# Kernel tuning notes

Hardware: AMD Instinct MI355X
Metric: run time of the kernel (lower is better)

Reference implementation:

```python
import jax, jax.numpy as jnp
import numpy as np


def _conv1x1(x, W, b):
    # 1x1 conv == per-pixel channel matmul: x [B,C,H,W], W [O,C], b [O]
    return jnp.einsum('bchw,oc->bohw', x, W) + b[None, :, None, None]


def setup_inputs() -> dict:
    key = jax.random.key(0)
    ks = jax.random.split(key, 9)
    B, C, H, W = 16, 512, 32, 32
    s = 1.0 / np.sqrt(C)
    inp = {
        'x': jax.random.normal(ks[0], (B, C, H, W), dtype=jnp.float32),
        'Wq': jax.random.normal(ks[1], (C, C), dtype=jnp.float32) * s,
        'bq': jax.random.normal(ks[2], (C,), dtype=jnp.float32) * 0.01,
        'Wk': jax.random.normal(ks[3], (C, C), dtype=jnp.float32) * s,
        'bk': jax.random.normal(ks[4], (C,), dtype=jnp.float32) * 0.01,
        'Wv': jax.random.normal(ks[5], (C, C), dtype=jnp.float32) * s,
        'bv': jax.random.normal(ks[6], (C,), dtype=jnp.float32) * 0.01,
        'Wo': jax.random.normal(ks[7], (C, C), dtype=jnp.float32) * s,
        'bo': jax.random.normal(ks[8], (C,), dtype=jnp.float32) * 0.01,
    }
    return inp


def reference(x, Wq, bq, Wk, bk, Wv, bv, Wo, bo):
    B, C, H, W = x.shape
    q = _conv1x1(x, Wq, bq)
    k = _conv1x1(x, Wk, bk)
    v = _conv1x1(x, Wv, bv)
    hw = H * W
    qf = q.reshape(B, C, hw)  # [B,C,HW]
    kf = k.reshape(B, C, hw)
    vf = v.reshape(B, C, hw)
    # scores[b,i,j] = sum_c q[b,c,i] * k[b,c,j], scaled by c^-0.5
    scores = jnp.einsum('bci,bcj->bij', qf, kf) * (C ** -0.5)
    attn = jax.nn.softmax(scores, axis=2)  # softmax over keys j
    # out[b,c,i] = sum_j v[b,c,j] * attn[b,i,j]
    out = jnp.einsum('bcj,bij->bci', vf, attn).reshape(B, C, H, W)
    out = _conv1x1(out, Wo, bo)
    return x + out
```

## Files before the change

### kernel.cpp

```cpp
#include <hip/hip_runtime.h>
#include <hip/hip_bf16.h>
#include <math.h>


typedef __bf16 bf16x8 __attribute__((ext_vector_type(8)));
typedef float  f32x16 __attribute__((ext_vector_type(16)));

__device__ __forceinline__ unsigned short f2bf(float f) {
    unsigned u = __float_as_uint(f);
    u += 0x7fff + ((u >> 16) & 1);
    return (unsigned short)(u >> 16);
}

__device__ __forceinline__ void gload_lds16(const void* g, void* l) {
    __builtin_amdgcn_global_load_lds(
        (const __attribute__((address_space(1))) void*)g,
        (__attribute__((address_space(3))) void*)l, 16, 0, 0);
}

struct GemmP {
    const unsigned short* A;
    const unsigned short* B;
    void* C;
    const float* bias;
    const float* resid;
    float* lsum;
    int M, N, K, ldA, ldB;
    long sA, sB, sC, sR;
    int ln_nn, ln_pb;
    float scale;
};

template<bool OUT_F32, int BIAS_MODE, bool RESID, int EXPM>
__device__ __forceinline__ void gemm_body(const GemmP p, int L,
                                          unsigned short* Als,
                                          unsigned short* Bls)
{
    const int xcd = L & 7;
    const int idx = L >> 3;
    const int bz  = xcd * 2 + (idx >> p.ln_pb);
    const int w   = idx & ((1 << p.ln_pb) - 1);
    const int m0  = (w >> p.ln_nn) << 7;
    const int n0  = (w & ((1 << p.ln_nn) - 1)) << 7;

    const unsigned short* A = p.A + bz * p.sA;
    const unsigned short* B = p.B + bz * p.sB;

    const int tid  = threadIdx.x;
    const int lane = tid & 63;
    const int wave = tid >> 6;
    const int wm   = wave >> 1;
    const int wn   = wave & 1;

    const int ar = lane >> 2;
    const int ak = (((lane & 3) ^ ((ar >> 1) & 3))) * 8;

    const unsigned short* agp = A + (long)(m0 + wave * 16 + ar) * p.ldA + ak;
    const unsigned short* bgp = B + (long)(n0 + wave * 16 + ar) * p.ldB + ak;
    const long aj = 64L * p.ldA;
    const long bj = 64L * p.ldB;

    unsigned short* al0  = Als + wave * 512;
    unsigned short* al0h = Als + (wave + 4) * 512;
    unsigned short* al1  = Als + 4096 + wave * 512;
    unsigned short* al1h = Als + 4096 + (wave + 4) * 512;
    unsigned short* bl0  = Bls + wave * 512;
    unsigned short* bl0h = Bls + (wave + 4) * 512;
    unsigned short* bl1  = Bls + 4096 + wave * 512;
    unsigned short* bl1h = Bls + 4096 + (wave + 4) * 512;

    const int ln31 = lane & 31;
    const int hi   = lane >> 5;
    const int swz  = ((ln31 >> 1) & 3) << 3;

    f32x16 acc[2][2] = {};

    for (int k0 = 0; k0 < p.K; k0 += 64) {
        gload_lds16(agp,           al0);
        gload_lds16(agp + aj,      al0h);
        gload_lds16(agp + 32,      al1);
        gload_lds16(agp + 32 + aj, al1h);
        gload_lds16(bgp,           bl0);
        gload_lds16(bgp + bj,      bl0h);
        gload_lds16(bgp + 32,      bl1);
        gload_lds16(bgp + 32 + bj, bl1h);
        agp += 64; bgp += 64;
        __syncthreads();

        #pragma unroll
        for (int pp = 0; pp < 2; ++pp) {
            const unsigned short* Ap = Als + pp * 4096;
            const unsigned short* Bp = Bls + pp * 4096;
            bf16x8 af[2][2], bfr[2][2];
            #pragma unroll
            for (int mt = 0; mt < 2; ++mt)
                #pragma unroll
                for (int ks = 0; ks < 2; ++ks)
                    af[mt][ks] = *(const bf16x8*)
                        &Ap[(wm * 64 + mt * 32 + ln31) * 32 +
                            ((ks * 16 + hi * 8) ^ swz)];
            #pragma unroll
            for (int nt = 0; nt < 2; ++nt)
                #pragma unroll
                for (int ks = 0; ks < 2; ++ks)
                    bfr[nt][ks] = *(const bf16x8*)
                        &Bp[(wn * 64 + nt * 32 + ln31) * 32 +
                            ((ks * 16 + hi * 8) ^ swz)];

            #pragma unroll
            for (int ks = 0; ks < 2; ++ks)
                #pragma unroll
                for (int mt = 0; mt < 2; ++mt)
                    #pragma unroll
                    for (int nt = 0; nt < 2; ++nt)
                        acc[mt][nt] = __builtin_amdgcn_mfma_f32_32x32x16_bf16(
                            af[mt][ks], bfr[nt][ks], acc[mt][nt], 0, 0, 0);
        }
        __syncthreads();
    }

    float* Cf = (float*)p.C + bz * p.sC;
    unsigned short* Ch = (unsigned short*)p.C + bz * p.sC;
    const float* resid = RESID ? (p.resid + bz * p.sR) : nullptr;
    const int N = p.N;

    if (EXPM == 1) {
        float* lrow = p.lsum + bz * (long)p.M;
        #pragma unroll
        for (int mt = 0; mt < 2; ++mt) {
            #pragma unroll
            for (int r = 0; r < 16; ++r) {
                const int row = m0 + wm * 64 + mt * 32 +
                                (r & 3) + 8 * (r >> 2) + 4 * hi;
                float rs = 0.0f;
                #pragma unroll
                for (int nt = 0; nt < 2; ++nt) {
                    const int col = n0 + wn * 64 + nt * 32 + ln31;
                    const float e = __expf(acc[mt][nt][r] * p.scale);
                    rs += e;
                    Ch[(long)row * N + col] = f2bf(e);
                }
                rs += __shfl_xor(rs, 1);
                rs += __shfl_xor(rs, 2);
                rs += __shfl_xor(rs, 4);
                rs += __shfl_xor(rs, 8);
                rs += __shfl_xor(rs, 16);
                if (ln31 == 0) atomicAdd(&lrow[row], rs);
            }
        }
    } else {
        #pragma unroll
        for (int mt = 0; mt < 2; ++mt) {
            float linv[16];
            if (EXPM == 2) {
                const float* lrow = p.lsum + bz * (long)p.M;
                #pragma unroll
                for (int r = 0; r < 16; ++r)
                    linv[r] = 1.0f / lrow[m0 + wm * 64 + mt * 32 +
                                          (r & 3) + 8 * (r >> 2) + 4 * hi];
            }
            #pragma unroll
            for (int nt = 0; nt < 2; ++nt) {
                const int col = n0 + wn * 64 + nt * 32 + ln31;
                const float bn = (BIAS_MODE == 2) ? p.bias[col] : 0.0f;
                #pragma unroll
                for (int r = 0; r < 16; ++r) {
                    const int row = m0 + wm * 64 + mt * 32 +
                                    (r & 3) + 8 * (r >> 2) + 4 * hi;
                    float val = acc[mt][nt][r] + bn;
                    if (BIAS_MODE == 1) val += p.bias[row];
                    if (EXPM == 2) val *= linv[r];
                    const long o = (long)row * N + col;
                    if (RESID) val += resid[o];
                    if (OUT_F32) Cf[o] = val;
                    else         Ch[o] = f2bf(val);
                }
            }
        }
    }
}

template<bool OUT_F32, int BIAS_MODE, bool RESID, int EXPM>
__global__ __launch_bounds__(256) void gemm_bt_mfma(GemmP p)
{
    __shared__ unsigned short Als[2 * 4096];
    __shared__ unsigned short Bls[2 * 4096];
    gemm_body<OUT_F32, BIAS_MODE, RESID, EXPM>(p, blockIdx.x, Als, Bls);
}

__global__ __launch_bounds__(256) void gemm_qkv_fused(GemmP pqk, GemmP pv, int split)
{
    __shared__ unsigned short Als[2 * 4096];
    __shared__ unsigned short Bls[2 * 4096];
    if ((int)blockIdx.x < split)
        gemm_body<false, 2, false, 0>(pqk, blockIdx.x, Als, Bls);
    else
        gemm_body<false, 1, false, 0>(pv, blockIdx.x - split, Als, Bls);
}

__global__ __launch_bounds__(256) void prep_all(
    const float* __restrict__ x, unsigned short* __restrict__ xT,
    const float* __restrict__ Wq, const float* __restrict__ Wk,
    const float* __restrict__ Wv, const float* __restrict__ Wo,
    const float* __restrict__ bq, const float* __restrict__ bk,
    unsigned short* __restrict__ Wb, float* __restrict__ biasqk,
    float* __restrict__ lsum)
{
    const int b = blockIdx.x;
    const int t = threadIdx.x;
    if (b < 8192) {
        __shared__ float tl[32][33];
        const int batch = b >> 9;
        const int rem = b & 511;
        const int p0 = (rem & 31) * 32;
        const int c0 = (rem >> 5) * 32;
        const float* xb = x + (long)batch * 524288;
        unsigned short* xTb = xT + (long)batch * 524288;
        const int tx = t & 31;
        const int ty = t >> 5;
        #pragma unroll
        for (int i = 0; i < 4; ++i)
            tl[ty + 8 * i][tx] = xb[(long)(c0 + ty + 8 * i) * 1024 + p0 + tx];
        __syncthreads();
        #pragma unroll
        for (int i = 0; i < 4; ++i)
            xTb[(long)(p0 + ty + 8 * i) * 512 + c0 + tx] = f2bf(tl[tx][ty + 8 * i]);
    } else if (b < 9216) {
        const int wb = b - 8192;
        const float* srcs[4] = {Wq, Wk, Wv, Wo};
        const float* s = srcs[wb >> 8];
        unsigned short* d = Wb + (long)(wb >> 8) * 262144;
        const int i = ((wb & 255) * 256 + t) * 4;
        const float4 f = *(const float4*)(s + i);
        ushort4 h;
        h.x = f2bf(f.x); h.y = f2bf(f.y); h.z = f2bf(f.z); h.w = f2bf(f.w);
        *(ushort4*)(d + i) = h;
    } else {
        biasqk[t]       = bq[t];
        biasqk[256 + t] = bq[256 + t];
        biasqk[512 + t] = bk[t];
        biasqk[768 + t] = bk[256 + t];
        #pragma unroll
        for (int i = 0; i < 64; ++i) lsum[i * 256 + t] = 0.0f;
    }
}

extern "C" void kernel_launch(void* const* d_in, const int* in_sizes, int n_in,
                              void* d_out, int out_size, void* d_ws, size_t ws_size,
                              hipStream_t stream)
{
    const float* x  = (const float*)d_in[0];
    const float* Wq = (const float*)d_in[1];
    const float* bq = (const float*)d_in[2];
    const float* Wk = (const float*)d_in[3];
    const float* bk = (const float*)d_in[4];
    const float* Wv = (const float*)d_in[5];
    const float* bv = (const float*)d_in[6];
    const float* Wo = (const float*)d_in[7];
    const float* bo = (const float*)d_in[8];
    float* out = (float*)d_out;

    const int Bn = 16, C = 512, HW = 1024;
    const long CHW = (long)C * HW;
    const long SHW = (long)HW * HW;

    unsigned short* xT   = (unsigned short*)d_ws;
    unsigned short* qkT  = xT + Bn * CHW;
    unsigned short* vB   = qkT + Bn * SHW;
    unsigned short* expS = vB + Bn * CHW;
    unsigned short* Wb   = expS + Bn * SHW;
    float* biasqk = (float*)(Wb + 4 * 262144);
    float* lsum   = biasqk + 1024;
    unsigned short* OT = xT;

    unsigned short* Wvb = Wb + 2 * 262144;
    unsigned short* Wob = Wb + 3 * 262144;

    const dim3 blk(256);
    const float scale = 0.044194173824159216f;

    prep_all<<<dim3(9217), blk, 0, stream>>>(x, xT, Wq, Wk, Wv, Wo, bq, bk,
                                             Wb, biasqk, lsum);

    GemmP pqk = { xT, Wb, qkT, biasqk, nullptr, nullptr,
                  HW, 2 * C, C, C, C, CHW, 0, SHW, 0, 3, 6, 0.0f };
    GemmP pv  = { Wvb, xT, vB, bv, nullptr, nullptr,
                  C, HW, C, C, C, 0, CHW, CHW, 0, 3, 5, 0.0f };
    gemm_qkv_fused<<<dim3(1536), blk, 0, stream>>>(pqk, pv, 1024);

    GemmP ps  = { qkT, qkT + C, expS, nullptr, nullptr, lsum,
                  HW, HW, C, 2 * C, 2 * C, SHW, SHW, SHW, 0, 3, 6, scale };
    gemm_bt_mfma<false, 0, false, 1><<<dim3(1024), blk, 0, stream>>>(ps);

    GemmP po  = { expS, vB, OT, nullptr, nullptr, lsum,
                  HW, C, HW, HW, HW, SHW, CHW, CHW, 0, 2, 5, 0.0f };
    gemm_bt_mfma<false, 0, false, 2><<<dim3(512), blk, 0, stream>>>(po);

    GemmP pout = { Wob, OT, out, bo, x, nullptr,
                   C, HW, C, C, C, 0, CHW, CHW, CHW, 3, 5, 0.0f };
    gemm_bt_mfma<true, 1, true, 0><<<dim3(512), blk, 0, stream>>>(pout);
}
```

Baseline: 227.0 us.

## Double-buffer LDS tiles to overlap global loads with MFMA compute

Replaces the load-then-compute loop over 64-wide K chunks with a ping-pong pipeline over 32-wide K chunks using the two LDS halves as buffers. The next chunk's global-to-LDS loads are issued before computing on the current one, so memory latency can hide behind MFMA work. The number of barriers per K element stays the same, but each step does half as much compute per barrier. The loop assumes K is a multiple of 64.

```diff
diff --git a/kernel.cpp b/kernel.cpp
--- a/kernel.cpp
+++ b/kernel.cpp
@@ -60,62 +60,64 @@
     const long aj = 64L * p.ldA;
     const long bj = 64L * p.ldB;
 
-    unsigned short* al0  = Als + wave * 512;
-    unsigned short* al0h = Als + (wave + 4) * 512;
-    unsigned short* al1  = Als + 4096 + wave * 512;
-    unsigned short* al1h = Als + 4096 + (wave + 4) * 512;
-    unsigned short* bl0  = Bls + wave * 512;
-    unsigned short* bl0h = Bls + (wave + 4) * 512;
-    unsigned short* bl1  = Bls + 4096 + wave * 512;
-    unsigned short* bl1h = Bls + 4096 + (wave + 4) * 512;
+    unsigned short* alw  = Als + wave * 512;
+    unsigned short* alwh = Als + (wave + 4) * 512;
+    unsigned short* blw  = Bls + wave * 512;
+    unsigned short* blwh = Bls + (wave + 4) * 512;
 
     const int ln31 = lane & 31;
     const int hi   = lane >> 5;
     const int swz  = ((ln31 >> 1) & 3) << 3;
+    const int aoff = (wm * 64 + ln31) * 32;
+    const int boff = (wn * 64 + ln31) * 32;
+    const int koff0 = (hi * 8) ^ swz;
+    const int koff1 = (16 + hi * 8) ^ swz;
 
     f32x16 acc[2][2] = {};
 
-    for (int k0 = 0; k0 < p.K; k0 += 64) {
-        gload_lds16(agp,           al0);
-        gload_lds16(agp + aj,      al0h);
-        gload_lds16(agp + 32,      al1);
-        gload_lds16(agp + 32 + aj, al1h);
-        gload_lds16(bgp,           bl0);
-        gload_lds16(bgp + bj,      bl0h);
-        gload_lds16(bgp + 32,      bl1);
-        gload_lds16(bgp + 32 + bj, bl1h);
-        agp += 64; bgp += 64;
-        __syncthreads();
-
-        #pragma unroll
-        for (int pp = 0; pp < 2; ++pp) {
-            const unsigned short* Ap = Als + pp * 4096;
-            const unsigned short* Bp = Bls + pp * 4096;
-            bf16x8 af[2][2], bfr[2][2];
+    const int nsteps = p.K >> 5;
+
+    auto STAGE = [&](int sel) {
+        gload_lds16(agp,      alw  + sel * 4096);
+        gload_lds16(agp + aj, alwh + sel * 4096);
+        gload_lds16(bgp,      blw  + sel * 4096);
+        gload_lds16(bgp + bj, blwh + sel * 4096);
+        agp += 32; bgp += 32;
+    };
+
+    auto COMPUTE = [&](int sel) {
+        const unsigned short* Ap = Als + sel * 4096;
+        const unsigned short* Bp = Bls + sel * 4096;
+        bf16x8 af[2][2], bfr[2][2];
+        #pragma unroll
+        for (int mt = 0; mt < 2; ++mt) {
+            af[mt][0] = *(const bf16x8*)&Ap[aoff + mt * 1024 + koff0];
+            af[mt][1] = *(const bf16x8*)&Ap[aoff + mt * 1024 + koff1];
+        }
+        #pragma unroll
+        for (int nt = 0; nt < 2; ++nt) {
+            bfr[nt][0] = *(const bf16x8*)&Bp[boff + nt * 1024 + koff0];
+            bfr[nt][1] = *(const bf16x8*)&Bp[boff + nt * 1024 + koff1];
+        }
+        #pragma unroll
+        for (int ks = 0; ks < 2; ++ks)
             #pragma unroll
             for (int mt = 0; mt < 2; ++mt)
                 #pragma unroll
-                for (int ks = 0; ks < 2; ++ks)
-                    af[mt][ks] = *(const bf16x8*)
-                        &Ap[(wm * 64 + mt * 32 + ln31) * 32 +
-                            ((ks * 16 + hi * 8) ^ swz)];
-            #pragma unroll
-            for (int nt = 0; nt < 2; ++nt)
-                #pragma unroll
-                for (int ks = 0; ks < 2; ++ks)
-                    bfr[nt][ks] = *(const bf16x8*)
-                        &Bp[(wn * 64 + nt * 32 + ln31) * 32 +
-                            ((ks * 16 + hi * 8) ^ swz)];
-
-            #pragma unroll
-            for (int ks = 0; ks < 2; ++ks)
-                #pragma unroll
-                for (int mt = 0; mt < 2; ++mt)
-                    #pragma unroll
-                    for (int nt = 0; nt < 2; ++nt)
-                        acc[mt][nt] = __builtin_amdgcn_mfma_f32_32x32x16_bf16(
-                            af[mt][ks], bfr[nt][ks], acc[mt][nt], 0, 0, 0);
-        }
+                for (int nt = 0; nt < 2; ++nt)
+                    acc[mt][nt] = __builtin_amdgcn_mfma_f32_32x32x16_bf16(
+                        af[mt][ks], bfr[nt][ks], acc[mt][nt], 0, 0, 0);
+    };
+
+    STAGE(0);
+    __syncthreads();
+
+    for (int t = 0; t < nsteps; t += 2) {
+        STAGE(1);
+        COMPUTE(0);
+        __syncthreads();
+        if (t + 2 < nsteps) STAGE(0);
+        COMPUTE(1);
         __syncthreads();
     }
 
```

Measured after the change: 241.3 us. +6.3%, slower.
